# Optimization experiments

Measured on AMD Instinct MI355X. Metric: run time of the kernel, lower is better.

The kernel has to match this reference:

```python
import jax, jax.numpy as jnp
import numpy as np

N, S, Q, E, H, D, F, L = 512, 90, 90, 256, 8, 32, 1024, 3  # batch, kv_len, q_len, embed, heads, head_dim, ffn, layers
POS_VOCAB = 90


def setup_inputs() -> dict:
    key = jax.random.key(0)
    ks = jax.random.split(key, 16)
    rn = lambda k, shp, s=0.05: (jax.random.normal(k, shp, jnp.float32) * s)
    return dict(
        x=jax.random.normal(ks[0], (N, S, E), jnp.float32),
        q=jax.random.normal(ks[1], (N, Q, E), jnp.float32),
        positions=jax.random.randint(ks[2], (N, S), 0, POS_VOCAB),
        pos_emb=rn(ks[3], (POS_VOCAB, E), 1.0),
        # per-head-dim Q/K/V projections, SHARED across heads (as in the torch module)
        Wq=rn(ks[4], (L, D, D)), Wk=rn(ks[5], (L, D, D)), Wv=rn(ks[6], (L, D, D)),
        Wo=rn(ks[7], (L, E, E)), bo=jnp.zeros((L, E), jnp.float32),
        g1=jnp.ones((L, E), jnp.float32), b1=jnp.zeros((L, E), jnp.float32),
        g2=jnp.ones((L, E), jnp.float32), b2=jnp.zeros((L, E), jnp.float32),
        Wf1=rn(ks[8], (L, E, F)), bf1=jnp.zeros((L, F), jnp.float32),
        Wf2=rn(ks[9], (L, F, E)), bf2=jnp.zeros((L, E), jnp.float32),
        Wc1=rn(ks[10], (E, 8), 0.1), bc1=jnp.zeros((8,), jnp.float32),
        Wc2=rn(ks[11], (8, 8), 0.1), bc2=jnp.zeros((8,), jnp.float32),
        Wc3=rn(ks[12], (8, 2), 0.1), bc3=jnp.zeros((2,), jnp.float32),
    )


def _ln(x, g, b, eps=1e-5):
    m = jnp.mean(x, -1, keepdims=True)
    v = jnp.mean((x - m) ** 2, -1, keepdims=True)
    return (x - m) * jax.lax.rsqrt(v + eps) * g + b


def _attn(v_in, k_in, q_in, Wv, Wk, Wq, Wo, bo):
    n, kl, _ = k_in.shape
    ql = q_in.shape[1]
    v = jnp.einsum('nkhd,de->nkhe', v_in.reshape(n, kl, H, D), Wv)
    k = jnp.einsum('nkhd,de->nkhe', k_in.reshape(n, kl, H, D), Wk)
    qh = jnp.einsum('nqhd,de->nqhe', q_in.reshape(n, ql, H, D), Wq)
    # note: scale is 1/sqrt(embed_size) as in the original, not 1/sqrt(head_dim)
    att = jax.nn.softmax(jnp.einsum('nqhd,nkhd->nhqk', qh, k) / jnp.sqrt(jnp.float32(E)), axis=-1)
    o = jnp.einsum('nhqk,nkhd->nqhd', att, v).reshape(n, ql, E)
    return o @ Wo + bo


def reference(x, q, positions, pos_emb, Wq, Wk, Wv, Wo, bo, g1, b1, g2, b2,
              Wf1, bf1, Wf2, bf2, Wc1, bc1, Wc2, bc2, Wc3, bc3):
    out = x + pos_emb[positions]           # dropout = identity at eval
    for i in range(L):
        a = _attn(out, out, q, Wv[i], Wk[i], Wq[i], Wo[i], bo[i])
        h = _ln(a + q, g1[i], b1[i])       # residual uses the ORIGINAL q every layer
        f = jax.nn.relu(h @ Wf1[i] + bf1[i]) @ Wf2[i] + bf2[i]
        out = _ln(f + h, g2[i], b2[i])
    z = jnp.tanh(out @ Wc1 + bc1)
    z = jnp.tanh(z @ Wc2 + bc2)
    return jax.nn.sigmoid(z @ Wc3 + bc3)   # [N, Q, 2]
```

## Files before the change

### kernel.cpp

```cpp
#include <hip/hip_runtime.h>

typedef __bf16 bf16x8 __attribute__((ext_vector_type(8)));
typedef __bf16 bf16x4 __attribute__((ext_vector_type(4)));
typedef float f32x4 __attribute__((ext_vector_type(4)));
typedef unsigned short u16x8 __attribute__((ext_vector_type(8)));
typedef unsigned short u16x4 __attribute__((ext_vector_type(4)));

__device__ __forceinline__ unsigned short f2b(float f) {
    union { float f; unsigned int u; } v; v.f = f;
    unsigned int r = v.u + 0x7fffu + ((v.u >> 16) & 1u);
    return (unsigned short)(r >> 16);
}
__device__ __forceinline__ float b2f(unsigned short b) {
    union { unsigned int u; float f; } v; v.u = ((unsigned int)b) << 16;
    return v.f;
}

__device__ __forceinline__ void gll16(const unsigned short* g, unsigned short* l) {
    __builtin_amdgcn_global_load_lds(
        (const __attribute__((address_space(1))) unsigned int*)g,
        (__attribute__((address_space(3))) unsigned int*)l, 16, 0, 0);
}

__global__ __launch_bounds__(256) void prep_wfrag(
    const float* __restrict__ W, unsigned short* __restrict__ dst, int K, int NN)
{
    int k0 = blockIdx.x * 32, n0 = blockIdx.y * 16;
    int KS = K >> 5;
    size_t fbase = ((size_t)(n0 >> 4) * KS + (k0 >> 5)) * 512;
    for (int p = threadIdx.x; p < 512; p += 256) {
        int e = p & 7, lane = p >> 3;
        int n = lane & 15, k = ((lane >> 4) << 3) + e;
        dst[fbase + p] = f2b(W[(size_t)(k0 + k) * NN + n0 + n]);
    }
}

__global__ __launch_bounds__(256) void prep_wT(
    const float* __restrict__ Wq, const float* __restrict__ Wk, const float* __restrict__ Wv,
    unsigned short* __restrict__ wT)
{
    int l = blockIdx.x / 3, w = blockIdx.x % 3;
    const float* src = (w == 0 ? Wq : w == 1 ? Wk : Wv) + (size_t)l * 1024;
    unsigned short* dst = wT + ((size_t)l * 3 + w) * 1024;
    float scale = (w == 0) ? 0.0625f : 1.0f;
    int t = threadIdx.x;
    f32x4 v = *(const f32x4*)&src[t * 4];
    int d = (t * 4) >> 5, j0 = (t * 4) & 31;
    #pragma unroll
    for (int e = 0; e < 4; e++)
        dst[(j0 + e) * 32 + d] = f2b(v[e] * scale);
}

__global__ __launch_bounds__(256) void add_posemb_q(
    const float* __restrict__ x, const int* __restrict__ pos,
    const float* __restrict__ pe, const float* __restrict__ q,
    unsigned short* __restrict__ cur, unsigned short* __restrict__ qb)
{
    size_t row = blockIdx.x;
    int t = threadIdx.x;
    int p = pos[row];
    cur[row * 256 + t] = f2b(x[row * 256 + t] + pe[(size_t)p * 256 + t]);
    qb[row * 256 + t] = f2b(q[row * 256 + t]);
}

__global__ __launch_bounds__(384, 2) void attn_kernel(
    const unsigned short* __restrict__ cur, const unsigned short* __restrict__ qb,
    const unsigned short* __restrict__ wT,
    unsigned short* __restrict__ og)
{
    __shared__ __align__(16) unsigned short smem[96 * 104 + 96 * 32];
    unsigned short* qs = smem;
    unsigned short* ks = smem + 96 * 40;
    unsigned short* ps = smem;
    unsigned short* vs = smem + 96 * 104;

    int nh = blockIdx.x;
    int n = nh >> 3, h = nh & 7;
    int tid = threadIdx.x;
    int wave = tid >> 6, lane = tid & 63;
    int lr = lane & 15, lg = lane >> 4;
    int hiw = lane & 1;

    bf16x8 wq[2], wk[2], wv[2];
    #pragma unroll
    for (int ct = 0; ct < 2; ct++) {
        int o = (ct * 16 + lr) * 32 + lg * 8;
        wq[ct] = *(const bf16x8*)&wT[o];
        wk[ct] = *(const bf16x8*)&wT[1024 + o];
        wv[ct] = *(const bf16x8*)&wT[2048 + o];
    }

    {
        int tile = wave;
        int row = tile * 16 + lr;
        bf16x8 aq = {0,0,0,0,0,0,0,0}, ac = {0,0,0,0,0,0,0,0};
        if (row < 90) {
            size_t base = ((size_t)(n * 90 + row)) * 256 + h * 32 + lg * 8;
            aq = *(const bf16x8*)&qb[base];
            ac = *(const bf16x8*)&cur[base];
        }
        f32x4 zz = {0.f, 0.f, 0.f, 0.f};
        #pragma unroll
        for (int ct = 0; ct < 2; ct++) {
            f32x4 qc = __builtin_amdgcn_mfma_f32_16x16x32_bf16(aq, wq[ct], zz, 0, 0, 0);
            f32x4 kc = __builtin_amdgcn_mfma_f32_16x16x32_bf16(ac, wk[ct], zz, 0, 0, 0);
            f32x4 vc = __builtin_amdgcn_mfma_f32_16x16x32_bf16(ac, wv[ct], zz, 0, 0, 0);
            #pragma unroll
            for (int rr = 0; rr < 4; rr++) {
                float oq = __shfl_xor(qc[rr], 1);
                unsigned a16 = f2b(qc[rr]), o16 = f2b(oq);
                unsigned pk = hiw ? (o16 | (a16 << 16)) : (a16 | (o16 << 16));
                if ((rr >> 1) == hiw)
                    *(unsigned*)&qs[(tile * 16 + lg * 4 + rr) * 40 + ct * 16 + (lr & ~1)] = pk;

                float ok = __shfl_xor(kc[rr], 1);
                a16 = f2b(kc[rr]); o16 = f2b(ok);
                pk = hiw ? (o16 | (a16 << 16)) : (a16 | (o16 << 16));
                if ((rr >> 1) == hiw)
                    *(unsigned*)&ks[(tile * 16 + lg * 4 + rr) * 40 + ct * 16 + (lr & ~1)] = pk;

                float ov = __shfl_xor(vc[rr], 1);
                a16 = f2b(vc[rr]); o16 = f2b(ov);
                pk = hiw ? (o16 | (a16 << 16)) : (a16 | (o16 << 16));
                if ((rr >> 1) == hiw)
                    *(unsigned*)&vs[(tile * 4 + lg) * 128 + ct * 64 + rr * 16 + (lr & ~1)] = pk;
            }
        }
    }
    __syncthreads();

    f32x4 c[6];
    {
        bf16x8 aq = *(const bf16x8*)&qs[(wave * 16 + lr) * 40 + lg * 8];
        #pragma unroll
        for (int j = 0; j < 6; j++) {
            bf16x8 bk = *(const bf16x8*)&ks[(j * 16 + lr) * 40 + lg * 8];
            f32x4 z = {0.f, 0.f, 0.f, 0.f};
            c[j] = __builtin_amdgcn_mfma_f32_16x16x32_bf16(aq, bk, z, 0, 0, 0);
        }
    }
    if (lr >= 10) { c[5][0] = -1e30f; c[5][1] = -1e30f; c[5][2] = -1e30f; c[5][3] = -1e30f; }

    #pragma unroll
    for (int rr = 0; rr < 4; rr++) {
        float m = c[0][rr];
        #pragma unroll
        for (int j = 1; j < 6; j++) m = fmaxf(m, c[j][rr]);
        m = fmaxf(m, __shfl_xor(m, 1));
        m = fmaxf(m, __shfl_xor(m, 2));
        m = fmaxf(m, __shfl_xor(m, 4));
        m = fmaxf(m, __shfl_xor(m, 8));
        float sum = 0.f;
        #pragma unroll
        for (int j = 0; j < 6; j++) {
            float e = __expf(c[j][rr] - m);
            c[j][rr] = e;
            sum += e;
        }
        sum += __shfl_xor(sum, 1);
        sum += __shfl_xor(sum, 2);
        sum += __shfl_xor(sum, 4);
        sum += __shfl_xor(sum, 8);
        float inv = 1.f / sum;
        #pragma unroll
        for (int j = 0; j < 6; j++) c[j][rr] *= inv;
    }
    __syncthreads();

    {
        int row_base = wave * 16 + lg * 4;
        #pragma unroll
        for (int j = 0; j < 6; j++) {
            #pragma unroll
            for (int rr = 0; rr < 4; rr++) {
                float oth = __shfl_xor(c[j][rr], 1);
                unsigned int own16 = f2b(c[j][rr]), oth16 = f2b(oth);
                unsigned int pk = hiw ? (oth16 | (own16 << 16)) : (own16 | (oth16 << 16));
                if ((rr >> 1) == hiw)
                    *(unsigned int*)&ps[(row_base + rr) * 104 + j * 16 + (lr & ~1)] = pk;
            }
        }
    }
    __syncthreads();

    {
        unsigned vbase = (unsigned)(size_t)&vs[0];
        f32x4 oc0 = {0.f,0.f,0.f,0.f}, oc1 = {0.f,0.f,0.f,0.f};
        #pragma unroll
        for (int s = 0; s < 3; s++) {
            bf16x8 ap = *(const bf16x8*)&ps[(wave * 16 + lr) * 104 + s * 32 + lg * 8];
            unsigned ta = vbase + (unsigned)((8 * s + 2 * lg) * 256) + (unsigned)(lr * 8);
            bf16x4 b0a, b0b, b1a, b1b;
            asm volatile(
                "ds_read_b64_tr_b16 %0, %4\n\t"
                "ds_read_b64_tr_b16 %1, %4 offset:256\n\t"
                "ds_read_b64_tr_b16 %2, %4 offset:128\n\t"
                "ds_read_b64_tr_b16 %3, %4 offset:384\n\t"
                "s_waitcnt lgkmcnt(0)"
                : "=&v"(b0a), "=&v"(b0b), "=&v"(b1a), "=&v"(b1b)
                : "v"(ta) : "memory");
            __builtin_amdgcn_sched_barrier(0);
            bf16x8 bv0, bv1;
            #pragma unroll
            for (int e = 0; e < 4; e++) {
                bv0[e] = b0a[e]; bv0[4 + e] = b0b[e];
                bv1[e] = b1a[e]; bv1[4 + e] = b1b[e];
            }
            oc0 = __builtin_amdgcn_mfma_f32_16x16x32_bf16(ap, bv0, oc0, 0, 0, 0);
            oc1 = __builtin_amdgcn_mfma_f32_16x16x32_bf16(ap, bv1, oc1, 0, 0, 0);
        }
        #pragma unroll
        for (int rr = 0; rr < 4; rr++) {
            int row = wave * 16 + lg * 4 + rr;
            if (row < 90) {
                size_t base = ((size_t)(n * 90 + row)) * 256 + h * 32;
                og[base + lr]      = f2b(oc0[rr]);
                og[base + 16 + lr] = f2b(oc1[rr]);
            }
        }
    }
}

__global__ __launch_bounds__(256, 4) void gemm_wo(
    const unsigned short* __restrict__ A, const unsigned short* __restrict__ Bf,
    const float* __restrict__ bias,
    const unsigned short* __restrict__ res, const float* __restrict__ gw,
    const float* __restrict__ bw,
    unsigned short* __restrict__ C)
{
    __shared__ __align__(16) unsigned short As[8 * 2048];
    __shared__ float ssum[64 * 4], ssq[64 * 4];

    int bx = blockIdx.x;
    bx = (bx & 7) * 90 + (bx >> 3);
    int ra0 = bx * 64;

    int tid = threadIdx.x;
    int wave = tid >> 6, lane = tid & 63;
    int wc = wave;
    int lr = lane & 15, lg = lane >> 4;
    int rsub = lane >> 2, sp = lane & 3;
    int nt0 = wc * 4;

    f32x4 acc[4][4];
    #pragma unroll
    for (int i = 0; i < 4; i++)
        #pragma unroll
        for (int j = 0; j < 4; j++)
            acc[i][j] = (f32x4){0.f, 0.f, 0.f, 0.f};

    #pragma unroll
    for (int kw = 0; kw < 8; kw++) {
        int r = wave * 16 + rsub;
        int sl = sp ^ ((r >> 1) & 3);
        gll16(&A[(size_t)(ra0 + r) * 256 + kw * 32 + sl * 8], &As[kw * 2048 + wave * 512]);
    }
    bf16x8 xwA[4], xwB[4];
    #pragma unroll
    for (int j = 0; j < 4; j++)
        xwA[j] = *(const bf16x8*)&Bf[((size_t)(nt0 + j) * 8 + 0) * 512 + lane * 8];
    asm volatile("s_waitcnt vmcnt(4)" ::: "memory");
    __builtin_amdgcn_s_barrier();
    __builtin_amdgcn_sched_barrier(0);

    #pragma unroll 1
    for (int it = 0; it < 8; it += 2) {
        if (it + 1 < 8) {
            #pragma unroll
            for (int j = 0; j < 4; j++)
                xwB[j] = *(const bf16x8*)&Bf[((size_t)(nt0 + j) * 8 + it + 1) * 512 + lane * 8];
        }
        {
            bf16x8 ya[4];
            #pragma unroll
            for (int i = 0; i < 4; i++) {
                int mm = i * 16 + lr;
                ya[i] = *(const bf16x8*)&As[it * 2048 + mm * 32 + (lg ^ ((mm >> 1) & 3)) * 8];
            }
            #pragma unroll
            for (int i = 0; i < 4; i++)
                #pragma unroll
                for (int j = 0; j < 4; j++)
                    acc[i][j] = __builtin_amdgcn_mfma_f32_16x16x32_bf16(xwA[j], ya[i], acc[i][j], 0, 0, 0);
        }
        if (it + 2 < 8) {
            #pragma unroll
            for (int j = 0; j < 4; j++)
                xwA[j] = *(const bf16x8*)&Bf[((size_t)(nt0 + j) * 8 + it + 2) * 512 + lane * 8];
        }
        {
            bf16x8 ya[4];
            #pragma unroll
            for (int i = 0; i < 4; i++) {
                int mm = i * 16 + lr;
                ya[i] = *(const bf16x8*)&As[(it + 1) * 2048 + mm * 32 + (lg ^ ((mm >> 1) & 3)) * 8];
            }
            #pragma unroll
            for (int i = 0; i < 4; i++)
                #pragma unroll
                for (int j = 0; j < 4; j++)
                    acc[i][j] = __builtin_amdgcn_mfma_f32_16x16x32_bf16(xwB[j], ya[i], acc[i][j], 0, 0, 0);
        }
    }

    float s1[4] = {0.f,0.f,0.f,0.f}, sq[4] = {0.f,0.f,0.f,0.f};
    #pragma unroll
    for (int i = 0; i < 4; i++) {
        int row = ra0 + i * 16 + lr;
        #pragma unroll
        for (int j = 0; j < 4; j++) {
            int ncol = wc * 64 + j * 16 + lg * 4;
            f32x4 bv = *(const f32x4*)&bias[ncol];
            u16x4 rv = *(const u16x4*)&res[(size_t)row * 256 + ncol];
            #pragma unroll
            for (int rr = 0; rr < 4; rr++) {
                acc[i][j][rr] += bv[rr] + b2f(rv[rr]);
                s1[i] += acc[i][j][rr];
                sq[i] += acc[i][j][rr] * acc[i][j][rr];
            }
        }
    }
    #pragma unroll
    for (int i = 0; i < 4; i++) {
        s1[i] += __shfl_xor(s1[i], 16);  s1[i] += __shfl_xor(s1[i], 32);
        sq[i] += __shfl_xor(sq[i], 16);  sq[i] += __shfl_xor(sq[i], 32);
        if (lg == 0) {
            int rb = i * 16 + lr;
            ssum[rb * 4 + wc] = s1[i];
            ssq[rb * 4 + wc]  = sq[i];
        }
    }
    __syncthreads();
    #pragma unroll
    for (int i = 0; i < 4; i++) {
        int rb = i * 16 + lr;
        float ts = 0.f, tq = 0.f;
        #pragma unroll
        for (int w = 0; w < 4; w++) { ts += ssum[rb * 4 + w]; tq += ssq[rb * 4 + w]; }
        float mean = ts * (1.f / 256.f);
        float var = tq * (1.f / 256.f) - mean * mean;
        float inv = rsqrtf(var + 1e-5f);
        int row = ra0 + rb;
        #pragma unroll
        for (int j = 0; j < 4; j++) {
            int ncol = wc * 64 + j * 16 + lg * 4;
            f32x4 gv = *(const f32x4*)&gw[ncol];
            f32x4 bv = *(const f32x4*)&bw[ncol];
            u16x4 ov;
            #pragma unroll
            for (int rr = 0; rr < 4; rr++)
                ov[rr] = f2b((acc[i][j][rr] - mean) * inv * gv[rr] + bv[rr]);
            *(u16x4*)&C[(size_t)row * 256 + ncol] = ov;
        }
    }
}

__global__ __launch_bounds__(256, 2) void ffn_fused2(
    const unsigned short* __restrict__ A,
    const unsigned short* __restrict__ W1F, const float* __restrict__ bf1,
    const unsigned short* __restrict__ W2F, const float* __restrict__ bf2,
    const float* __restrict__ g2, const float* __restrict__ b2,
    unsigned short* __restrict__ C)
{
    __shared__ __align__(16) unsigned short As[8 * 2048];
    __shared__ __align__(16) unsigned short f1s[8 * 2048];
    __shared__ float ssum[64 * 4], ssq[64 * 4];

    int bx = blockIdx.x;
    bx = (bx & 7) * 90 + (bx >> 3);
    int ra0 = bx * 64;

    int tid = threadIdx.x;
    int wave = tid >> 6, lane = tid & 63;
    int wc = wave;
    int lr = lane & 15, lg = lane >> 4;
    int rsub = lane >> 2, sp = lane & 3;

    #pragma unroll
    for (int kw = 0; kw < 8; kw++) {
        int r = wave * 16 + rsub;
        int sl = sp ^ ((r >> 1) & 3);
        gll16(&A[(size_t)(ra0 + r) * 256 + kw * 32 + sl * 8], &As[kw * 2048 + wave * 512]);
    }
    asm volatile("s_waitcnt vmcnt(0)" ::: "memory");
    __builtin_amdgcn_s_barrier();
    __builtin_amdgcn_sched_barrier(0);

    f32x4 acc2[4][4];
    #pragma unroll
    for (int i = 0; i < 4; i++)
        #pragma unroll
        for (int j = 0; j < 4; j++)
            acc2[i][j] = (f32x4){0.f, 0.f, 0.f, 0.f};

    #pragma unroll 1
    for (int fc = 0; fc < 4; fc++) {
        f32x4 acc1[4][4];
        #pragma unroll
        for (int i = 0; i < 4; i++)
            #pragma unroll
            for (int j = 0; j < 4; j++)
                acc1[i][j] = (f32x4){0.f, 0.f, 0.f, 0.f};

        int ntb1 = fc * 16 + wc * 4;
        bf16x8 xa[4], xb[4];
        #pragma unroll
        for (int j = 0; j < 4; j++)
            xa[j] = *(const bf16x8*)&W1F[((size_t)(ntb1 + j) * 8 + 0) * 512 + lane * 8];
        #pragma unroll
        for (int k2 = 0; k2 < 8; k2 += 2) {
            if (k2 + 1 < 8) {
                #pragma unroll
                for (int j = 0; j < 4; j++)
                    xb[j] = *(const bf16x8*)&W1F[((size_t)(ntb1 + j) * 8 + k2 + 1) * 512 + lane * 8];
            }
            {
                bf16x8 ya[4];
                #pragma unroll
                for (int i = 0; i < 4; i++) {
                    int mm = i * 16 + lr;
                    ya[i] = *(const bf16x8*)&As[k2 * 2048 + mm * 32 + (lg ^ ((mm >> 1) & 3)) * 8];
                }
                #pragma unroll
                for (int i = 0; i < 4; i++)
                    #pragma unroll
                    for (int j = 0; j < 4; j++)
                        acc1[i][j] = __builtin_amdgcn_mfma_f32_16x16x32_bf16(xa[j], ya[i], acc1[i][j], 0, 0, 0);
            }
            if (k2 + 2 < 8) {
                #pragma unroll
                for (int j = 0; j < 4; j++)
                    xa[j] = *(const bf16x8*)&W1F[((size_t)(ntb1 + j) * 8 + k2 + 2) * 512 + lane * 8];
            }
            {
                bf16x8 ya[4];
                #pragma unroll
                for (int i = 0; i < 4; i++) {
                    int mm = i * 16 + lr;
                    ya[i] = *(const bf16x8*)&As[(k2 + 1) * 2048 + mm * 32 + (lg ^ ((mm >> 1) & 3)) * 8];
                }
                #pragma unroll
                for (int i = 0; i < 4; i++)
                    #pragma unroll
                    for (int j = 0; j < 4; j++)
                        acc1[i][j] = __builtin_amdgcn_mfma_f32_16x16x32_bf16(xb[j], ya[i], acc1[i][j], 0, 0, 0);
            }
        }

        #pragma unroll
        for (int i = 0; i < 4; i++) {
            int row = i * 16 + lr;
            #pragma unroll
            for (int j = 0; j < 4; j++) {
                int ncol = wc * 64 + j * 16 + lg * 4;
                f32x4 bv = *(const f32x4*)&bf1[fc * 256 + ncol];
                int win = ncol >> 5, cw = ncol & 31;
                int p = (cw >> 3) ^ ((row >> 1) & 3);
                u16x4 ov;
                #pragma unroll
                for (int rr = 0; rr < 4; rr++)
                    ov[rr] = f2b(fmaxf(acc1[i][j][rr] + bv[rr], 0.f));
                *(u16x4*)&f1s[win * 2048 + row * 32 + p * 8 + (cw & 7)] = ov;
            }
        }
        __syncthreads();

        int ntb2 = wc * 4;
        #pragma unroll
        for (int j = 0; j < 4; j++)
            xa[j] = *(const bf16x8*)&W2F[((size_t)(ntb2 + j) * 32 + fc * 8 + 0) * 512 + lane * 8];
        #pragma unroll
        for (int k2 = 0; k2 < 8; k2 += 2) {
            if (k2 + 1 < 8) {
                #pragma unroll
                for (int j = 0; j < 4; j++)
                    xb[j] = *(const bf16x8*)&W2F[((size_t)(ntb2 + j) * 32 + fc * 8 + k2 + 1) * 512 + lane * 8];
            }
            {
                bf16x8 ya[4];
                #pragma unroll
                for (int i = 0; i < 4; i++) {
                    int mm = i * 16 + lr;
                    ya[i] = *(const bf16x8*)&f1s[k2 * 2048 + mm * 32 + (lg ^ ((mm >> 1) & 3)) * 8];
                }
                #pragma unroll
                for (int i = 0; i < 4; i++)
                    #pragma unroll
                    for (int j = 0; j < 4; j++)
                        acc2[i][j] = __builtin_amdgcn_mfma_f32_16x16x32_bf16(xa[j], ya[i], acc2[i][j], 0, 0, 0);
            }
            if (k2 + 2 < 8) {
                #pragma unroll
                for (int j = 0; j < 4; j++)
                    xa[j] = *(const bf16x8*)&W2F[((size_t)(ntb2 + j) * 32 + fc * 8 + k2 + 2) * 512 + lane * 8];
            }
            {
                bf16x8 ya[4];
                #pragma unroll
                for (int i = 0; i < 4; i++) {
                    int mm = i * 16 + lr;
                    ya[i] = *(const bf16x8*)&f1s[(k2 + 1) * 2048 + mm * 32 + (lg ^ ((mm >> 1) & 3)) * 8];
                }
                #pragma unroll
                for (int i = 0; i < 4; i++)
                    #pragma unroll
                    for (int j = 0; j < 4; j++)
                        acc2[i][j] = __builtin_amdgcn_mfma_f32_16x16x32_bf16(xb[j], ya[i], acc2[i][j], 0, 0, 0);
            }
        }
        __syncthreads();
    }

    float s1[4] = {0.f,0.f,0.f,0.f}, sq[4] = {0.f,0.f,0.f,0.f};
    #pragma unroll
    for (int i = 0; i < 4; i++) {
        int row = i * 16 + lr;
        #pragma unroll
        for (int j = 0; j < 4; j++) {
            int ncol = wc * 64 + j * 16 + lg * 4;
            f32x4 bv = *(const f32x4*)&bf2[ncol];
            int win = ncol >> 5, cw = ncol & 31;
            int p = (cw >> 3) ^ ((row >> 1) & 3);
            u16x4 rv = *(const u16x4*)&As[win * 2048 + row * 32 + p * 8 + (cw & 7)];
            #pragma unroll
            for (int rr = 0; rr < 4; rr++) {
                acc2[i][j][rr] += bv[rr] + b2f(rv[rr]);
                s1[i] += acc2[i][j][rr];
                sq[i] += acc2[i][j][rr] * acc2[i][j][rr];
            }
        }
    }
    #pragma unroll
    for (int i = 0; i < 4; i++) {
        s1[i] += __shfl_xor(s1[i], 16);  s1[i] += __shfl_xor(s1[i], 32);
        sq[i] += __shfl_xor(sq[i], 16);  sq[i] += __shfl_xor(sq[i], 32);
        if (lg == 0) {
            int rb = i * 16 + lr;
            ssum[rb * 4 + wc] = s1[i];
            ssq[rb * 4 + wc]  = sq[i];
        }
    }
    __syncthreads();
    #pragma unroll
    for (int i = 0; i < 4; i++) {
        int rb = i * 16 + lr;
        float ts = 0.f, tq = 0.f;
        #pragma unroll
        for (int w = 0; w < 4; w++) { ts += ssum[rb * 4 + w]; tq += ssq[rb * 4 + w]; }
        float mean = ts * (1.f / 256.f);
        float var = tq * (1.f / 256.f) - mean * mean;
        float inv = rsqrtf(var + 1e-5f);
        int row = ra0 + rb;
        #pragma unroll
        for (int j = 0; j < 4; j++) {
            int ncol = wc * 64 + j * 16 + lg * 4;
            f32x4 gv = *(const f32x4*)&g2[ncol];
            f32x4 bv = *(const f32x4*)&b2[ncol];
            u16x4 ov;
            #pragma unroll
            for (int rr = 0; rr < 4; rr++)
                ov[rr] = f2b((acc2[i][j][rr] - mean) * inv * gv[rr] + bv[rr]);
            *(u16x4*)&C[(size_t)row * 256 + ncol] = ov;
        }
    }
}

__global__ __launch_bounds__(256) void classifier(
    const unsigned short* __restrict__ xin,
    const float* __restrict__ Wc1, const float* __restrict__ bc1,
    const float* __restrict__ Wc2, const float* __restrict__ bc2,
    const float* __restrict__ Wc3, const float* __restrict__ bc3,
    float* __restrict__ out)
{
    __shared__ float w1[256][9];
    __shared__ float w2[64], b2s[8], w3[16], b3s[2], b1s[8];
    int t = threadIdx.x;
    #pragma unroll
    for (int i = 0; i < 8; i++) {
        int idx = t + i * 256;
        w1[idx >> 3][idx & 7] = Wc1[idx];
    }
    if (t < 64) w2[t] = Wc2[t];
    if (t < 16) w3[t] = Wc3[t];
    if (t < 8) { b2s[t] = bc2[t]; b1s[t] = bc1[t]; }
    if (t < 2) b3s[t] = bc3[t];
    __syncthreads();
    int g = t >> 3, m = t & 7;
    size_t row = (size_t)blockIdx.x * 32 + g;
    float z[8] = {0.f,0.f,0.f,0.f,0.f,0.f,0.f,0.f};
    const unsigned short* xr = xin + row * 256 + m * 32;
    #pragma unroll
    for (int cidx = 0; cidx < 4; cidx++) {
        u16x8 xv = *(const u16x8*)&xr[cidx * 8];
        #pragma unroll
        for (int e = 0; e < 8; e++) {
            float xf = b2f(xv[e]);
            int ei = m * 32 + cidx * 8 + e;
            #pragma unroll
            for (int j = 0; j < 8; j++) z[j] = fmaf(xf, w1[ei][j], z[j]);
        }
    }
    #pragma unroll
    for (int d = 1; d < 8; d <<= 1)
        #pragma unroll
        for (int j = 0; j < 8; j++) z[j] += __shfl_xor(z[j], d);
    float z1[8], z2[8];
    #pragma unroll
    for (int j = 0; j < 8; j++) z1[j] = tanhf(z[j] + b1s[j]);
    #pragma unroll
    for (int j2 = 0; j2 < 8; j2++) {
        float sacc = b2s[j2];
        #pragma unroll
        for (int j = 0; j < 8; j++) sacc = fmaf(z1[j], w2[j * 8 + j2], sacc);
        z2[j2] = tanhf(sacc);
    }
    if (m < 2) {
        float sacc = b3s[m];
        #pragma unroll
        for (int j = 0; j < 8; j++) sacc = fmaf(z2[j], w3[j * 2 + m], sacc);
        out[row * 2 + m] = 1.f / (1.f + __expf(-sacc));
    }
}

extern "C" void kernel_launch(void* const* d_in, const int* in_sizes, int n_in,
                              void* d_out, int out_size, void* d_ws, size_t ws_size,
                              hipStream_t stream) {
    const float* x        = (const float*)d_in[0];
    const float* q        = (const float*)d_in[1];
    const int*   positions= (const int*)d_in[2];
    const float* pos_emb  = (const float*)d_in[3];
    const float* Wq       = (const float*)d_in[4];
    const float* Wk       = (const float*)d_in[5];
    const float* Wv       = (const float*)d_in[6];
    const float* Wo       = (const float*)d_in[7];
    const float* bo       = (const float*)d_in[8];
    const float* g1       = (const float*)d_in[9];
    const float* b1       = (const float*)d_in[10];
    const float* g2       = (const float*)d_in[11];
    const float* b2       = (const float*)d_in[12];
    const float* Wf1      = (const float*)d_in[13];
    const float* bf1      = (const float*)d_in[14];
    const float* Wf2      = (const float*)d_in[15];
    const float* bf2      = (const float*)d_in[16];
    const float* Wc1      = (const float*)d_in[17];
    const float* bc1      = (const float*)d_in[18];
    const float* Wc2      = (const float*)d_in[19];
    const float* bc2      = (const float*)d_in[20];
    const float* Wc3      = (const float*)d_in[21];
    const float* bc3      = (const float*)d_in[22];
    float* out = (float*)d_out;

    const int R = 512 * 90;
    char* ws = (char*)d_ws;
    size_t off = 0;
    auto alloc = [&](size_t bytes) -> void* {
        void* p = ws + off;
        off += (bytes + 255) & ~(size_t)255;
        return p;
    };
    unsigned short* cur = (unsigned short*)alloc((size_t)R * 256 * 2);
    unsigned short* qb  = (unsigned short*)alloc((size_t)R * 256 * 2);
    unsigned short* qho = (unsigned short*)alloc((size_t)R * 256 * 2);
    unsigned short* WoF = (unsigned short*)alloc((size_t)3 * 256 * 256 * 2);
    unsigned short* W1F = (unsigned short*)alloc((size_t)3 * 1024 * 256 * 2);
    unsigned short* W2F = (unsigned short*)alloc((size_t)3 * 256 * 1024 * 2);
    unsigned short* WTqkv = (unsigned short*)alloc((size_t)3 * 3 * 1024 * 2);

    for (int l = 0; l < 3; l++) {
        prep_wfrag<<<dim3(8, 16),  256, 0, stream>>>(Wo  + (size_t)l*256*256,  WoF + (size_t)l*256*256,  256, 256);
        prep_wfrag<<<dim3(8, 64),  256, 0, stream>>>(Wf1 + (size_t)l*256*1024, W1F + (size_t)l*1024*256, 256, 1024);
        prep_wfrag<<<dim3(32, 16), 256, 0, stream>>>(Wf2 + (size_t)l*1024*256, W2F + (size_t)l*256*1024, 1024, 256);
    }
    prep_wT<<<9, 256, 0, stream>>>(Wq, Wk, Wv, WTqkv);
    add_posemb_q<<<R, 256, 0, stream>>>(x, positions, pos_emb, q, cur, qb);

    for (int l = 0; l < 3; l++) {
        attn_kernel<<<512 * 8, 384, 0, stream>>>(cur, qb, WTqkv + (size_t)l * 3 * 1024, qho);
        gemm_wo<<<dim3(720), 256, 0, stream>>>(
            qho, WoF + (size_t)l*256*256, bo + l*256,
            qb, g1 + l*256, b1 + l*256, qho);
        ffn_fused2<<<dim3(720), 256, 0, stream>>>(
            qho, W1F + (size_t)l*1024*256, bf1 + l*1024,
            W2F + (size_t)l*256*1024, bf2 + l*256,
            g2 + l*256, b2 + l*256, cur);
    }
    classifier<<<R / 32, 256, 0, stream>>>(cur, Wc1, bc1, Wc2, bc2, Wc3, bc3, out);
}
```

Measured before the change: 488.8 us.

## Fuse Wo projection and LayerNorm1 into the FFN kernel

Merges the output-projection GEMM with residual and LayerNorm into the fused FFN kernel. The normalized h tile stays in shared memory and feeds FF1 directly, and the shared-memory buffers are reused between stages. This removes one kernel launch per layer plus the global write and re-read of the intermediate h tensor. In exchange, each block runs a longer serial chain with extra barriers, and the FF1 output now reuses the input buffer, which needs an additional sync inside the chunk loop.

```diff
diff --git a/kernel.cpp b/kernel.cpp
--- a/kernel.cpp
+++ b/kernel.cpp
@@ -221,149 +221,17 @@
     }
 }
 
-__global__ __launch_bounds__(256, 4) void gemm_wo(
-    const unsigned short* __restrict__ A, const unsigned short* __restrict__ Bf,
-    const float* __restrict__ bias,
-    const unsigned short* __restrict__ res, const float* __restrict__ gw,
-    const float* __restrict__ bw,
-    unsigned short* __restrict__ C)
-{
-    __shared__ __align__(16) unsigned short As[8 * 2048];
-    __shared__ float ssum[64 * 4], ssq[64 * 4];
-
-    int bx = blockIdx.x;
-    bx = (bx & 7) * 90 + (bx >> 3);
-    int ra0 = bx * 64;
-
-    int tid = threadIdx.x;
-    int wave = tid >> 6, lane = tid & 63;
-    int wc = wave;
-    int lr = lane & 15, lg = lane >> 4;
-    int rsub = lane >> 2, sp = lane & 3;
-    int nt0 = wc * 4;
-
-    f32x4 acc[4][4];
-    #pragma unroll
-    for (int i = 0; i < 4; i++)
-        #pragma unroll
-        for (int j = 0; j < 4; j++)
-            acc[i][j] = (f32x4){0.f, 0.f, 0.f, 0.f};
-
-    #pragma unroll
-    for (int kw = 0; kw < 8; kw++) {
-        int r = wave * 16 + rsub;
-        int sl = sp ^ ((r >> 1) & 3);
-        gll16(&A[(size_t)(ra0 + r) * 256 + kw * 32 + sl * 8], &As[kw * 2048 + wave * 512]);
-    }
-    bf16x8 xwA[4], xwB[4];
-    #pragma unroll
-    for (int j = 0; j < 4; j++)
-        xwA[j] = *(const bf16x8*)&Bf[((size_t)(nt0 + j) * 8 + 0) * 512 + lane * 8];
-    asm volatile("s_waitcnt vmcnt(4)" ::: "memory");
-    __builtin_amdgcn_s_barrier();
-    __builtin_amdgcn_sched_barrier(0);
-
-    #pragma unroll 1
-    for (int it = 0; it < 8; it += 2) {
-        if (it + 1 < 8) {
-            #pragma unroll
-            for (int j = 0; j < 4; j++)
-                xwB[j] = *(const bf16x8*)&Bf[((size_t)(nt0 + j) * 8 + it + 1) * 512 + lane * 8];
-        }
-        {
-            bf16x8 ya[4];
-            #pragma unroll
-            for (int i = 0; i < 4; i++) {
-                int mm = i * 16 + lr;
-                ya[i] = *(const bf16x8*)&As[it * 2048 + mm * 32 + (lg ^ ((mm >> 1) & 3)) * 8];
-            }
-            #pragma unroll
-            for (int i = 0; i < 4; i++)
-                #pragma unroll
-                for (int j = 0; j < 4; j++)
-                    acc[i][j] = __builtin_amdgcn_mfma_f32_16x16x32_bf16(xwA[j], ya[i], acc[i][j], 0, 0, 0);
-        }
-        if (it + 2 < 8) {
-            #pragma unroll
-            for (int j = 0; j < 4; j++)
-                xwA[j] = *(const bf16x8*)&Bf[((size_t)(nt0 + j) * 8 + it + 2) * 512 + lane * 8];
-        }
-        {
-            bf16x8 ya[4];
-            #pragma unroll
-            for (int i = 0; i < 4; i++) {
-                int mm = i * 16 + lr;
-                ya[i] = *(const bf16x8*)&As[(it + 1) * 2048 + mm * 32 + (lg ^ ((mm >> 1) & 3)) * 8];
-            }
-            #pragma unroll
-            for (int i = 0; i < 4; i++)
-                #pragma unroll
-                for (int j = 0; j < 4; j++)
-                    acc[i][j] = __builtin_amdgcn_mfma_f32_16x16x32_bf16(xwB[j], ya[i], acc[i][j], 0, 0, 0);
-        }
-    }
-
-    float s1[4] = {0.f,0.f,0.f,0.f}, sq[4] = {0.f,0.f,0.f,0.f};
-    #pragma unroll
-    for (int i = 0; i < 4; i++) {
-        int row = ra0 + i * 16 + lr;
-        #pragma unroll
-        for (int j = 0; j < 4; j++) {
-            int ncol = wc * 64 + j * 16 + lg * 4;
-            f32x4 bv = *(const f32x4*)&bias[ncol];
-            u16x4 rv = *(const u16x4*)&res[(size_t)row * 256 + ncol];
-            #pragma unroll
-            for (int rr = 0; rr < 4; rr++) {
-                acc[i][j][rr] += bv[rr] + b2f(rv[rr]);
-                s1[i] += acc[i][j][rr];
-                sq[i] += acc[i][j][rr] * acc[i][j][rr];
-            }
-        }
-    }
-    #pragma unroll
-    for (int i = 0; i < 4; i++) {
-        s1[i] += __shfl_xor(s1[i], 16);  s1[i] += __shfl_xor(s1[i], 32);
-        sq[i] += __shfl_xor(sq[i], 16);  sq[i] += __shfl_xor(sq[i], 32);
-        if (lg == 0) {
-            int rb = i * 16 + lr;
-            ssum[rb * 4 + wc] = s1[i];
-            ssq[rb * 4 + wc]  = sq[i];
-        }
-    }
-    __syncthreads();
-    #pragma unroll
-    for (int i = 0; i < 4; i++) {
-        int rb = i * 16 + lr;
-        float ts = 0.f, tq = 0.f;
-        #pragma unroll
-        for (int w = 0; w < 4; w++) { ts += ssum[rb * 4 + w]; tq += ssq[rb * 4 + w]; }
-        float mean = ts * (1.f / 256.f);
-        float var = tq * (1.f / 256.f) - mean * mean;
-        float inv = rsqrtf(var + 1e-5f);
-        int row = ra0 + rb;
-        #pragma unroll
-        for (int j = 0; j < 4; j++) {
-            int ncol = wc * 64 + j * 16 + lg * 4;
-            f32x4 gv = *(const f32x4*)&gw[ncol];
-            f32x4 bv = *(const f32x4*)&bw[ncol];
-            u16x4 ov;
-            #pragma unroll
-            for (int rr = 0; rr < 4; rr++)
-                ov[rr] = f2b((acc[i][j][rr] - mean) * inv * gv[rr] + bv[rr]);
-            *(u16x4*)&C[(size_t)row * 256 + ncol] = ov;
-        }
-    }
-}
-
-__global__ __launch_bounds__(256, 2) void ffn_fused2(
+__global__ __launch_bounds__(256, 2) void wo_ffn_fused(
     const unsigned short* __restrict__ A,
+    const unsigned short* __restrict__ WoFl, const float* __restrict__ bo,
+    const unsigned short* __restrict__ qb, const float* __restrict__ g1, const float* __restrict__ b1,
     const unsigned short* __restrict__ W1F, const float* __restrict__ bf1,
     const unsigned short* __restrict__ W2F, const float* __restrict__ bf2,
     const float* __restrict__ g2, const float* __restrict__ b2,
     unsigned short* __restrict__ C)
 {
     __shared__ __align__(16) unsigned short As[8 * 2048];
-    __shared__ __align__(16) unsigned short f1s[8 * 2048];
+    __shared__ __align__(16) unsigned short hs[8 * 2048];
     __shared__ float ssum[64 * 4], ssq[64 * 4];
 
     int bx = blockIdx.x;
@@ -386,33 +254,25 @@
     __builtin_amdgcn_s_barrier();
     __builtin_amdgcn_sched_barrier(0);
 
-    f32x4 acc2[4][4];
-    #pragma unroll
-    for (int i = 0; i < 4; i++)
+    {
+        f32x4 acc[4][4];
+        #pragma unroll
+        for (int i = 0; i < 4; i++)
+            #pragma unroll
+            for (int j = 0; j < 4; j++)
+                acc[i][j] = (f32x4){0.f, 0.f, 0.f, 0.f};
+
+        int nt0 = wc * 4;
+        bf16x8 xa[4], xb[4];
         #pragma unroll
         for (int j = 0; j < 4; j++)
-            acc2[i][j] = (f32x4){0.f, 0.f, 0.f, 0.f};
-
-    #pragma unroll 1
-    for (int fc = 0; fc < 4; fc++) {
-        f32x4 acc1[4][4];
-        #pragma unroll
-        for (int i = 0; i < 4; i++)
-            #pragma unroll
-            for (int j = 0; j < 4; j++)
-                acc1[i][j] = (f32x4){0.f, 0.f, 0.f, 0.f};
-
-        int ntb1 = fc * 16 + wc * 4;
-        bf16x8 xa[4], xb[4];
-        #pragma unroll
-        for (int j = 0; j < 4; j++)
-            xa[j] = *(const bf16x8*)&W1F[((size_t)(ntb1 + j) * 8 + 0) * 512 + lane * 8];
+            xa[j] = *(const bf16x8*)&WoFl[((size_t)(nt0 + j) * 8 + 0) * 512 + lane * 8];
         #pragma unroll
         for (int k2 = 0; k2 < 8; k2 += 2) {
             if (k2 + 1 < 8) {
                 #pragma unroll
                 for (int j = 0; j < 4; j++)
-                    xb[j] = *(const bf16x8*)&W1F[((size_t)(ntb1 + j) * 8 + k2 + 1) * 512 + lane * 8];
+                    xb[j] = *(const bf16x8*)&WoFl[((size_t)(nt0 + j) * 8 + k2 + 1) * 512 + lane * 8];
             }
             {
                 bf16x8 ya[4];
@@ -425,12 +285,12 @@
                 for (int i = 0; i < 4; i++)
                     #pragma unroll
                     for (int j = 0; j < 4; j++)
-                        acc1[i][j] = __builtin_amdgcn_mfma_f32_16x16x32_bf16(xa[j], ya[i], acc1[i][j], 0, 0, 0);
+                        acc[i][j] = __builtin_amdgcn_mfma_f32_16x16x32_bf16(xa[j], ya[i], acc[i][j], 0, 0, 0);
             }
             if (k2 + 2 < 8) {
                 #pragma unroll
                 for (int j = 0; j < 4; j++)
-                    xa[j] = *(const bf16x8*)&W1F[((size_t)(ntb1 + j) * 8 + k2 + 2) * 512 + lane * 8];
+                    xa[j] = *(const bf16x8*)&WoFl[((size_t)(nt0 + j) * 8 + k2 + 2) * 512 + lane * 8];
             }
             {
                 bf16x8 ya[4];
@@ -443,10 +303,127 @@
                 for (int i = 0; i < 4; i++)
                     #pragma unroll
                     for (int j = 0; j < 4; j++)
+                        acc[i][j] = __builtin_amdgcn_mfma_f32_16x16x32_bf16(xb[j], ya[i], acc[i][j], 0, 0, 0);
+            }
+        }
+
+        float s1[4] = {0.f,0.f,0.f,0.f}, sq[4] = {0.f,0.f,0.f,0.f};
+        #pragma unroll
+        for (int i = 0; i < 4; i++) {
+            int row = ra0 + i * 16 + lr;
+            #pragma unroll
+            for (int j = 0; j < 4; j++) {
+                int ncol = wc * 64 + j * 16 + lg * 4;
+                f32x4 bv = *(const f32x4*)&bo[ncol];
+                u16x4 rv = *(const u16x4*)&qb[(size_t)row * 256 + ncol];
+                #pragma unroll
+                for (int rr = 0; rr < 4; rr++) {
+                    acc[i][j][rr] += bv[rr] + b2f(rv[rr]);
+                    s1[i] += acc[i][j][rr];
+                    sq[i] += acc[i][j][rr] * acc[i][j][rr];
+                }
+            }
+        }
+        #pragma unroll
+        for (int i = 0; i < 4; i++) {
+            s1[i] += __shfl_xor(s1[i], 16);  s1[i] += __shfl_xor(s1[i], 32);
+            sq[i] += __shfl_xor(sq[i], 16);  sq[i] += __shfl_xor(sq[i], 32);
+            if (lg == 0) {
+                int rb = i * 16 + lr;
+                ssum[rb * 4 + wc] = s1[i];
+                ssq[rb * 4 + wc]  = sq[i];
+            }
+        }
+        __syncthreads();
+        #pragma unroll
+        for (int i = 0; i < 4; i++) {
+            int rb = i * 16 + lr;
+            float ts = 0.f, tq = 0.f;
+            #pragma unroll
+            for (int w = 0; w < 4; w++) { ts += ssum[rb * 4 + w]; tq += ssq[rb * 4 + w]; }
+            float mean = ts * (1.f / 256.f);
+            float var = tq * (1.f / 256.f) - mean * mean;
+            float inv = rsqrtf(var + 1e-5f);
+            #pragma unroll
+            for (int j = 0; j < 4; j++) {
+                int ncol = wc * 64 + j * 16 + lg * 4;
+                f32x4 gv = *(const f32x4*)&g1[ncol];
+                f32x4 bv = *(const f32x4*)&b1[ncol];
+                int row = i * 16 + lr;
+                int win = ncol >> 5, cw = ncol & 31;
+                int p = (cw >> 3) ^ ((row >> 1) & 3);
+                u16x4 ov;
+                #pragma unroll
+                for (int rr = 0; rr < 4; rr++)
+                    ov[rr] = f2b((acc[i][j][rr] - mean) * inv * gv[rr] + bv[rr]);
+                *(u16x4*)&hs[win * 2048 + row * 32 + p * 8 + (cw & 7)] = ov;
+            }
+        }
+    }
+    __syncthreads();
+
+    f32x4 acc2[4][4];
+    #pragma unroll
+    for (int i = 0; i < 4; i++)
+        #pragma unroll
+        for (int j = 0; j < 4; j++)
+            acc2[i][j] = (f32x4){0.f, 0.f, 0.f, 0.f};
+
+    #pragma unroll 1
+    for (int fc = 0; fc < 4; fc++) {
+        f32x4 acc1[4][4];
+        #pragma unroll
+        for (int i = 0; i < 4; i++)
+            #pragma unroll
+            for (int j = 0; j < 4; j++)
+                acc1[i][j] = (f32x4){0.f, 0.f, 0.f, 0.f};
+
+        int ntb1 = fc * 16 + wc * 4;
+        bf16x8 xa[4], xb[4];
+        #pragma unroll
+        for (int j = 0; j < 4; j++)
+            xa[j] = *(const bf16x8*)&W1F[((size_t)(ntb1 + j) * 8 + 0) * 512 + lane * 8];
+        #pragma unroll
+        for (int k2 = 0; k2 < 8; k2 += 2) {
+            if (k2 + 1 < 8) {
+                #pragma unroll
+                for (int j = 0; j < 4; j++)
+                    xb[j] = *(const bf16x8*)&W1F[((size_t)(ntb1 + j) * 8 + k2 + 1) * 512 + lane * 8];
+            }
+            {
+                bf16x8 ya[4];
+                #pragma unroll
+                for (int i = 0; i < 4; i++) {
+                    int mm = i * 16 + lr;
+                    ya[i] = *(const bf16x8*)&hs[k2 * 2048 + mm * 32 + (lg ^ ((mm >> 1) & 3)) * 8];
+                }
+                #pragma unroll
+                for (int i = 0; i < 4; i++)
+                    #pragma unroll
+                    for (int j = 0; j < 4; j++)
+                        acc1[i][j] = __builtin_amdgcn_mfma_f32_16x16x32_bf16(xa[j], ya[i], acc1[i][j], 0, 0, 0);
+            }
+            if (k2 + 2 < 8) {
+                #pragma unroll
+                for (int j = 0; j < 4; j++)
+                    xa[j] = *(const bf16x8*)&W1F[((size_t)(ntb1 + j) * 8 + k2 + 2) * 512 + lane * 8];
+            }
+            {
+                bf16x8 ya[4];
+                #pragma unroll
+                for (int i = 0; i < 4; i++) {
+                    int mm = i * 16 + lr;
+                    ya[i] = *(const bf16x8*)&hs[(k2 + 1) * 2048 + mm * 32 + (lg ^ ((mm >> 1) & 3)) * 8];
+                }
+                #pragma unroll
+                for (int i = 0; i < 4; i++)
+                    #pragma unroll
+                    for (int j = 0; j < 4; j++)
                         acc1[i][j] = __builtin_amdgcn_mfma_f32_16x16x32_bf16(xb[j], ya[i], acc1[i][j], 0, 0, 0);
             }
         }
 
+        __syncthreads();
         #pragma unroll
         for (int i = 0; i < 4; i++) {
             int row = i * 16 + lr;
@@ -460,7 +437,7 @@
                 #pragma unroll
                 for (int rr = 0; rr < 4; rr++)
                     ov[rr] = f2b(fmaxf(acc1[i][j][rr] + bv[rr], 0.f));
-                *(u16x4*)&f1s[win * 2048 + row * 32 + p * 8 + (cw & 7)] = ov;
+                *(u16x4*)&As[win * 2048 + row * 32 + p * 8 + (cw & 7)] = ov;
             }
         }
         __syncthreads();
@@ -481,7 +458,7 @@
                 #pragma unroll
                 for (int i = 0; i < 4; i++) {
                     int mm = i * 16 + lr;
-                    ya[i] = *(const bf16x8*)&f1s[k2 * 2048 + mm * 32 + (lg ^ ((mm >> 1) & 3)) * 8];
+                    ya[i] = *(const bf16x8*)&As[k2 * 2048 + mm * 32 + (lg ^ ((mm >> 1) & 3)) * 8];
                 }
                 #pragma unroll
                 for (int i = 0; i < 4; i++)
@@ -499,7 +476,7 @@
                 #pragma unroll
                 for (int i = 0; i < 4; i++) {
                     int mm = i * 16 + lr;
-                    ya[i] = *(const bf16x8*)&f1s[(k2 + 1) * 2048 + mm * 32 + (lg ^ ((mm >> 1) & 3)) * 8];
+                    ya[i] = *(const bf16x8*)&As[(k2 + 1) * 2048 + mm * 32 + (lg ^ ((mm >> 1) & 3)) * 8];
                 }
                 #pragma unroll
                 for (int i = 0; i < 4; i++)
@@ -508,8 +485,8 @@
                         acc2[i][j] = __builtin_amdgcn_mfma_f32_16x16x32_bf16(xb[j], ya[i], acc2[i][j], 0, 0, 0);
             }
         }
-        __syncthreads();
-    }
+    }
+    __syncthreads();
 
     float s1[4] = {0.f,0.f,0.f,0.f}, sq[4] = {0.f,0.f,0.f,0.f};
     #pragma unroll
@@ -521,7 +498,7 @@
             f32x4 bv = *(const f32x4*)&bf2[ncol];
             int win = ncol >> 5, cw = ncol & 31;
             int p = (cw >> 3) ^ ((row >> 1) & 3);
-            u16x4 rv = *(const u16x4*)&As[win * 2048 + row * 32 + p * 8 + (cw & 7)];
+            u16x4 rv = *(const u16x4*)&hs[win * 2048 + row * 32 + p * 8 + (cw & 7)];
             #pragma unroll
             for (int rr = 0; rr < 4; rr++) {
                 acc2[i][j][rr] += bv[rr] + b2f(rv[rr]);
@@ -676,11 +653,10 @@
 
     for (int l = 0; l < 3; l++) {
         attn_kernel<<<512 * 8, 384, 0, stream>>>(cur, qb, WTqkv + (size_t)l * 3 * 1024, qho);
-        gemm_wo<<<dim3(720), 256, 0, stream>>>(
+        wo_ffn_fused<<<dim3(720), 256, 0, stream>>>(
             qho, WoF + (size_t)l*256*256, bo + l*256,
-            qb, g1 + l*256, b1 + l*256, qho);
-        ffn_fused2<<<dim3(720), 256, 0, stream>>>(
-            qho, W1F + (size_t)l*1024*256, bf1 + l*1024,
+            qb, g1 + l*256, b1 + l*256,
+            W1F + (size_t)l*1024*256, bf1 + l*1024,
             W2F + (size_t)l*256*1024, bf2 + l*256,
             g2 + l*256, b2 + l*256, cur);
     }
```

Result: faster. 463.7 us, median of 2 (-5.1%).
